# Optimization experiments

Hardware: AMD Instinct MI355X
Metric: run time of the kernel (lower is better)

The kernel has to match this reference:

```python
import jax, jax.numpy as jnp
import numpy as np

ALPHA = 0.99
EPS = 1e-6
EMA_INIT = 1e-4


def setup_inputs() -> dict:
    key = jax.random.key(0)
    k1, k2, k3 = jax.random.split(key, 3)
    B, T, C = 16, 8192, 512
    x = jax.random.normal(k1, (B, T, C), dtype=jnp.float32)
    gamma = jax.random.normal(k2, (1, C), dtype=jnp.float32)
    beta = jax.random.normal(k3, (1, C), dtype=jnp.float32)
    return {"x": x, "gamma": gamma, "beta": beta}


def _ema_scan(x2_scaled):
    """Parallel scan of ema_t = ALPHA*ema_{t-1} + x2_scaled_t along axis=1.
    Initial state EMA_INIT is folded into the first element."""
    B, T, C = x2_scaled.shape
    # fold init: b_1 <- b_1 + alpha * ema_init
    b = x2_scaled.at[:, 0, :].add(ALPHA * EMA_INIT)
    a = jnp.full((1, T, 1), ALPHA, dtype=x2_scaled.dtype)

    def combine(lhs, rhs):
        a1, b1 = lhs
        a2, b2 = rhs
        return a1 * a2, a2 * b1 + b2

    _, ema = jax.lax.associative_scan(combine, (a, b), axis=1)
    return ema  # (B, T, C)


def reference(x, gamma, beta):
    B, T, C = x.shape
    one_minus_a = jnp.asarray(1.0 - ALPHA, dtype=x.dtype)
    ema = _ema_scan(one_minus_a * x * x)  # (B,T,C)
    # bias correction: denom_t = 1 - alpha^t, t = 1..T
    k = jnp.arange(1, T + 1, dtype=x.dtype)
    denom = 1.0 - jnp.power(jnp.asarray(ALPHA, dtype=x.dtype), k)  # (T,)
    ema_hat = ema / (denom[None, :, None] + EPS)
    g = jnp.sqrt(ema_hat + EPS)  # (B,T,C)
    n = g / (jnp.mean(g, axis=-1, keepdims=True) + EPS)
    y = gamma * (x * n) + beta + x  # gamma/beta (1,C) broadcast over (B,T,C)
    return y
```

## Files before the change

kernel.cpp:

```cpp
#include <hip/hip_runtime.h>
#include <math.h>

constexpr int Bn = 16;
constexpr int Tn = 8192;
constexpr int Cn = 512;

constexpr float ALPHA    = 0.99f;
constexpr float ONE_M    = 0.01f;
constexpr float EPS      = 1e-6f;
constexpr float EMA_INIT = 1e-4f;

constexpr int L   = 128;
constexpr int NCH = Tn / L;
constexpr int G   = 8;

constexpr double cpow(double a, int n) { double r = 1.0; for (int i = 0; i < n; i++) r *= a; return r; }
constexpr float ALPHA_L  = (float)cpow(0.99, L);
constexpr float LN_ALPHA = (float)-0.010050335853501441;

#if __has_builtin(__builtin_amdgcn_rcpf)
__device__ inline float fast_rcp(float x) { return __builtin_amdgcn_rcpf(x); }
#else
__device__ inline float fast_rcp(float x) { return 1.0f / x; }
#endif

__global__ __launch_bounds__(512) void pass1_local(const float* __restrict__ x,
                                                   float* __restrict__ carry) {
    const int blk = blockIdx.x;
    const int b = blk >> 6;
    const int j = blk & (NCH - 1);
    const int c = threadIdx.x;

    const float* xp = x + ((size_t)(b * Tn + j * L)) * Cn + c;
    float s = 0.0f;
#pragma unroll 8
    for (int i = 0; i < L; i++) {
        float v = xp[(size_t)i * Cn];
        s = ALPHA * s + (ONE_M * v) * v;
    }
    carry[(size_t)blk * Cn + c] = s;
}

__global__ __launch_bounds__(256) void pass2_scan(const float* __restrict__ carry,
                                                  float* __restrict__ state) {
    const int idx = blockIdx.x * 256 + threadIdx.x;
    const int b = idx >> 9;
    const int c = idx & (Cn - 1);

    const size_t base = (size_t)b * NCH * Cn + c;
    float s = EMA_INIT;
#pragma unroll
    for (int j = 0; j < NCH; j++) {
        state[base + (size_t)j * Cn] = s;
        s = ALPHA_L * s + carry[base + (size_t)j * Cn];
    }
}

__global__ __launch_bounds__(512) void pass3_norm(const float* __restrict__ x,
                                                  const float* __restrict__ state,
                                                  const float* __restrict__ gamma,
                                                  const float* __restrict__ beta,
                                                  float* __restrict__ y) {
    __shared__ float part[2][G][8];

    const int blk  = blockIdx.x;
    const int b    = blk >> 6;
    const int j    = blk & (NCH - 1);
    const int c    = threadIdx.x;
    const int wave = c >> 6;
    const int lane = c & 63;

    float ema = state[(size_t)blk * Cn + c];
    const float gm = gamma[c];
    const float bt = beta[c];

    const int t0 = j * L;
    float p = __expf((float)t0 * LN_ALPHA);

    float xv[G], gv[G];
    for (int base = 0; base < L; base += G) {
        const int buf = (base / G) & 1;
        const float* xp = x + ((size_t)(b * Tn + t0 + base)) * Cn + c;

#pragma unroll
        for (int i = 0; i < G; i++) xv[i] = xp[(size_t)i * Cn];

#pragma unroll
        for (int i = 0; i < G; i++) {
            const float v = xv[i];
            ema = ALPHA * ema + (ONE_M * v) * v;
            p *= ALPHA;
            const float d = (1.0f - p) + EPS;
            const float gq = sqrtf(ema * fast_rcp(d) + EPS);
            gv[i] = gq;
            float r = gq;
#pragma unroll
            for (int off = 32; off; off >>= 1) r += __shfl_xor(r, off, 64);
            if (lane == 0) part[buf][i][wave] = r;
        }
        __syncthreads();
        float* yp = y + ((size_t)(b * Tn + t0 + base)) * Cn + c;
#pragma unroll
        for (int i = 0; i < G; i++) {
            const float4* p4 = (const float4*)part[buf][i];
            const float4 u = p4[0], w = p4[1];
            const float s8 = ((u.x + u.y) + (u.z + u.w)) + ((w.x + w.y) + (w.z + w.w));
            const float invm = fast_rcp(s8 * (1.0f / (float)Cn) + EPS);
            const float n = gv[i] * invm;
            const float out = gm * (xv[i] * n) + bt + xv[i];
            __builtin_nontemporal_store(out, yp + (size_t)i * Cn);
        }
    }
}

extern "C" void kernel_launch(void* const* d_in, const int* in_sizes, int n_in,
                              void* d_out, int out_size, void* d_ws, size_t ws_size,
                              hipStream_t stream) {
    const float* x     = (const float*)d_in[0];
    const float* gamma = (const float*)d_in[1];
    const float* beta  = (const float*)d_in[2];
    float* y = (float*)d_out;

    float* carry = (float*)d_ws;
    float* state = carry + (size_t)Bn * NCH * Cn;

    pass1_local<<<Bn * NCH, 512, 0, stream>>>(x, carry);
    pass2_scan<<<(Bn * Cn) / 256, 256, 0, stream>>>(carry, state);
    pass3_norm<<<Bn * NCH, 512, 0, stream>>>(x, state, gamma, beta, y);
}
```

Baseline: 518.2 us.

## Remap scan passes to one wave per short time chunk with vectorized rows

The chunk length drops from 128 to 16 time steps. Each wavefront now handles a whole 512-channel row, with 8 contiguous channels per lane loaded as float4. The per-row mean in the normalization pass becomes a single wave shuffle reduction, which removes the shared-memory partials and the block-wide barrier, and the next row is prefetched with non-temporal loads. In exchange, the carry and state buffers grow eightfold and the serial inter-chunk scan runs over 512 steps with only 8192 threads, which could become a latency bottleneck.

```diff
diff --git a/kernel.cpp b/kernel.cpp
--- a/kernel.cpp
+++ b/kernel.cpp
@@ -10,13 +10,12 @@
 constexpr float EPS      = 1e-6f;
 constexpr float EMA_INIT = 1e-4f;
 
-constexpr int L   = 128;
-constexpr int NCH = Tn / L;
-constexpr int G   = 8;
+constexpr int SC = 16;
+constexpr int NS = Tn / SC;
 
 constexpr double cpow(double a, int n) { double r = 1.0; for (int i = 0; i < n; i++) r *= a; return r; }
-constexpr float ALPHA_L  = (float)cpow(0.99, L);
-constexpr float LN_ALPHA = (float)-0.010050335853501441;
+constexpr float ALPHA_SC = (float)cpow(0.99, SC);
+constexpr float LN_ALPHA = -0.010050335853501441f;
 
 #if __has_builtin(__builtin_amdgcn_rcpf)
 __device__ inline float fast_rcp(float x) { return __builtin_amdgcn_rcpf(x); }
@@ -24,92 +23,124 @@
 __device__ inline float fast_rcp(float x) { return 1.0f / x; }
 #endif
 
-__global__ __launch_bounds__(512) void pass1_local(const float* __restrict__ x,
+typedef float f4 __attribute__((ext_vector_type(4)));
+
+__device__ inline f4 ld4(const float* p)  { return *(const f4*)p; }
+__device__ inline f4 ldnt4(const float* p){ return __builtin_nontemporal_load((const f4*)p); }
+__device__ inline void stnt4(float* p, f4 v) { __builtin_nontemporal_store(v, (f4*)p); }
+
+__global__ __launch_bounds__(256) void pass1_local(const float* __restrict__ x,
                                                    float* __restrict__ carry) {
-    const int blk = blockIdx.x;
-    const int b = blk >> 6;
-    const int j = blk & (NCH - 1);
-    const int c = threadIdx.x;
+    const int gw   = blockIdx.x * 4 + (threadIdx.x >> 6);
+    const int lane = threadIdx.x & 63;
+    const int b    = gw >> 9;
+    const int s    = gw & (NS - 1);
+    const int c0   = lane * 8;
 
-    const float* xp = x + ((size_t)(b * Tn + j * L)) * Cn + c;
-    float s = 0.0f;
-#pragma unroll 8
-    for (int i = 0; i < L; i++) {
-        float v = xp[(size_t)i * Cn];
-        s = ALPHA * s + (ONE_M * v) * v;
+    const float* xp = x + (size_t)(b * Tn + s * SC) * Cn + c0;
+
+    float acc[8];
+#pragma unroll
+    for (int k = 0; k < 8; k++) acc[k] = 0.0f;
+
+#pragma unroll
+    for (int i = 0; i < SC; i++) {
+        float v[8];
+        *(f4*)&v[0] = ld4(xp + (size_t)i * Cn);
+        *(f4*)&v[4] = ld4(xp + (size_t)i * Cn + 4);
+#pragma unroll
+        for (int k = 0; k < 8; k++)
+            acc[k] = fmaf(ALPHA, acc[k], (ONE_M * v[k]) * v[k]);
     }
-    carry[(size_t)blk * Cn + c] = s;
+
+    float* cp = carry + (size_t)(b * NS + s) * Cn + c0;
+    *(f4*)cp       = *(f4*)&acc[0];
+    *(f4*)(cp + 4) = *(f4*)&acc[4];
 }
 
-__global__ __launch_bounds__(256) void pass2_scan(const float* __restrict__ carry,
-                                                  float* __restrict__ state) {
-    const int idx = blockIdx.x * 256 + threadIdx.x;
+__global__ __launch_bounds__(64) void pass2_scan(const float* __restrict__ carry,
+                                                 float* __restrict__ state) {
+    const int idx = blockIdx.x * 64 + threadIdx.x;
     const int b = idx >> 9;
     const int c = idx & (Cn - 1);
 
-    const size_t base = (size_t)b * NCH * Cn + c;
+    const size_t base = (size_t)b * NS * Cn + c;
     float s = EMA_INIT;
-#pragma unroll
-    for (int j = 0; j < NCH; j++) {
+#pragma unroll 8
+    for (int j = 0; j < NS; j++) {
         state[base + (size_t)j * Cn] = s;
-        s = ALPHA_L * s + carry[base + (size_t)j * Cn];
+        s = fmaf(ALPHA_SC, s, carry[base + (size_t)j * Cn]);
     }
 }
 
-__global__ __launch_bounds__(512) void pass3_norm(const float* __restrict__ x,
+__global__ __launch_bounds__(256) void pass3_norm(const float* __restrict__ x,
                                                   const float* __restrict__ state,
                                                   const float* __restrict__ gamma,
                                                   const float* __restrict__ beta,
                                                   float* __restrict__ y) {
-    __shared__ float part[2][G][8];
+    const int gw   = blockIdx.x * 4 + (threadIdx.x >> 6);
+    const int lane = threadIdx.x & 63;
+    const int b    = gw >> 9;
+    const int s    = gw & (NS - 1);
+    const int c0   = lane * 8;
 
-    const int blk  = blockIdx.x;
-    const int b    = blk >> 6;
-    const int j    = blk & (NCH - 1);
-    const int c    = threadIdx.x;
-    const int wave = c >> 6;
-    const int lane = c & 63;
+    float ema[8], gm[8], bt[8];
+    {
+        const float* sp = state + (size_t)(b * NS + s) * Cn + c0;
+        *(f4*)&ema[0] = ld4(sp);
+        *(f4*)&ema[4] = ld4(sp + 4);
+        *(f4*)&gm[0]  = ld4(gamma + c0);
+        *(f4*)&gm[4]  = ld4(gamma + c0 + 4);
+        *(f4*)&bt[0]  = ld4(beta + c0);
+        *(f4*)&bt[4]  = ld4(beta + c0 + 4);
+    }
 
-    float ema = state[(size_t)blk * Cn + c];
-    const float gm = gamma[c];
-    const float bt = beta[c];
-
-    const int t0 = j * L;
+    const int t0 = s * SC;
     float p = __expf((float)t0 * LN_ALPHA);
 
-    float xv[G], gv[G];
-    for (int base = 0; base < L; base += G) {
-        const int buf = (base / G) & 1;
-        const float* xp = x + ((size_t)(b * Tn + t0 + base)) * Cn + c;
+    const float* xp = x + (size_t)(b * Tn + t0) * Cn + c0;
+    float*       yp = y + (size_t)(b * Tn + t0) * Cn + c0;
+
+    f4 xa = ldnt4(xp);
+    f4 xb = ldnt4(xp + 4);
 
 #pragma unroll
-        for (int i = 0; i < G; i++) xv[i] = xp[(size_t)i * Cn];
+    for (int i = 0; i < SC; i++) {
+        f4 na = xa, nb = xb;
+        if (i + 1 < SC) {
+            na = ldnt4(xp + (size_t)(i + 1) * Cn);
+            nb = ldnt4(xp + (size_t)(i + 1) * Cn + 4);
+        }
 
+        p *= ALPHA;
+        const float rd = fast_rcp((1.0f - p) + EPS);
+
+        float g[8];
+        float ls = 0.0f;
 #pragma unroll
-        for (int i = 0; i < G; i++) {
-            const float v = xv[i];
-            ema = ALPHA * ema + (ONE_M * v) * v;
-            p *= ALPHA;
-            const float d = (1.0f - p) + EPS;
-            const float gq = sqrtf(ema * fast_rcp(d) + EPS);
-            gv[i] = gq;
-            float r = gq;
+        for (int k = 0; k < 8; k++) {
+            const float v = (k < 4) ? xa[k] : xb[k - 4];
+            ema[k] = fmaf(ALPHA, ema[k], (ONE_M * v) * v);
+            g[k]   = sqrtf(fmaf(ema[k], rd, EPS));
+            ls    += g[k];
+        }
+
+        float r = ls;
 #pragma unroll
-            for (int off = 32; off; off >>= 1) r += __shfl_xor(r, off, 64);
-            if (lane == 0) part[buf][i][wave] = r;
+        for (int off = 32; off; off >>= 1) r += __shfl_xor(r, off, 64);
+        const float invm = fast_rcp(r * (1.0f / (float)Cn) + EPS);
+
+        f4 oa, ob;
+#pragma unroll
+        for (int k = 0; k < 8; k++) {
+            const float v   = (k < 4) ? xa[k] : xb[k - 4];
+            const float out = fmaf(gm[k], v * (g[k] * invm), bt[k] + v);
+            if (k < 4) oa[k] = out; else ob[k - 4] = out;
         }
-        __syncthreads();
-        float* yp = y + ((size_t)(b * Tn + t0 + base)) * Cn + c;
-#pragma unroll
-        for (int i = 0; i < G; i++) {
-            const float4* p4 = (const float4*)part[buf][i];
-            const float4 u = p4[0], w = p4[1];
-            const float s8 = ((u.x + u.y) + (u.z + u.w)) + ((w.x + w.y) + (w.z + w.w));
-            const float invm = fast_rcp(s8 * (1.0f / (float)Cn) + EPS);
-            const float n = gv[i] * invm;
-            const float out = gm * (xv[i] * n) + bt + xv[i];
-            __builtin_nontemporal_store(out, yp + (size_t)i * Cn);
-        }
+        stnt4(yp + (size_t)i * Cn, oa);
+        stnt4(yp + (size_t)i * Cn + 4, ob);
+
+        xa = na; xb = nb;
     }
 }
 
@@ -122,9 +153,9 @@
     float* y = (float*)d_out;
 
     float* carry = (float*)d_ws;
-    float* state = carry + (size_t)Bn * NCH * Cn;
+    float* state = carry + (size_t)Bn * NS * Cn;
 
-    pass1_local<<<Bn * NCH, 512, 0, stream>>>(x, carry);
-    pass2_scan<<<(Bn * Cn) / 256, 256, 0, stream>>>(carry, state);
-    pass3_norm<<<Bn * NCH, 512, 0, stream>>>(x, state, gamma, beta, y);
+    pass1_local<<<(Bn * NS) / 4, 256, 0, stream>>>(x, carry);
+    pass2_scan<<<(Bn * Cn) / 64, 64, 0, stream>>>(carry, state);
+    pass3_norm<<<(Bn * NS) / 4, 256, 0, stream>>>(x, state, gamma, beta, y);
 }
```

Result: slower. 618.2 us (+19.3%).
